# Kernel tuning notes

Measured on AMD Instinct MI355X. Metric: run time of the kernel, lower is better.

## Reference

```python
import jax, jax.numpy as jnp
import numpy as np
import math

B, S, D, M, H = 4, 2048, 1024, 512, 8
DK = M // H


def setup_inputs() -> dict:
    key = jax.random.key(0)
    ks = jax.random.split(key, 16)
    sd = lambda fan_in: 1.0 / math.sqrt(fan_in)
    inp = {
        'x': jax.random.normal(ks[0], (B, S, D), dtype=jnp.float32),
        'W_enc': jax.random.normal(ks[1], (D, M), dtype=jnp.float32) * sd(D),
        'b_enc': jnp.zeros((M,), jnp.float32),
        'Wq': jax.random.normal(ks[2], (M, M), dtype=jnp.float32) * sd(M),
        'bq': jnp.zeros((M,), jnp.float32),
        'Wk': jax.random.normal(ks[3], (M, M), dtype=jnp.float32) * sd(M),
        'bk': jnp.zeros((M,), jnp.float32),
        'Wv': jax.random.normal(ks[4], (M, M), dtype=jnp.float32) * sd(M),
        'bv': jnp.zeros((M,), jnp.float32),
        'Wo': jax.random.normal(ks[5], (M, M), dtype=jnp.float32) * sd(M),
        'bo': jnp.zeros((M,), jnp.float32),
        'ocr_bias': jnp.zeros((1, H, 1, 1), jnp.float32),  # learned, init zeros
        'W1': jax.random.normal(ks[6], (D + M, D), dtype=jnp.float32) * sd(D + M),
        'b1': jnp.zeros((D,), jnp.float32),
        'W2': jax.random.normal(ks[7], (D, D), dtype=jnp.float32) * sd(D),
        'b2': jnp.zeros((D,), jnp.float32),
        'ln_g': jnp.ones((D,), jnp.float32),
        'ln_b': jnp.zeros((D,), jnp.float32),
    }
    return inp


def _ocr_attention(m, Wq, bq, Wk, bk, Wv, bv, Wo, bo, ocr_bias):
    b, s, _ = m.shape
    q = (m @ Wq + bq).reshape(b, s, H, DK).transpose(0, 2, 1, 3)  # bhsd
    k = (m @ Wk + bk).reshape(b, s, H, DK).transpose(0, 2, 1, 3)
    v = (m @ Wv + bv).reshape(b, s, H, DK).transpose(0, 2, 1, 3)
    scores = jnp.einsum('bhqd,bhkd->bhqk', q, k) / math.sqrt(DK) + ocr_bias
    attn = jax.nn.softmax(scores, axis=-1)  # dropout is identity at eval
    ctx = jnp.einsum('bhqk,bhkd->bhqd', attn, v)
    ctx = ctx.transpose(0, 2, 1, 3).reshape(b, s, M)
    return ctx @ Wo + bo


def _layernorm(h, g, bta, eps=1e-5):
    mu = jnp.mean(h, axis=-1, keepdims=True)
    var = jnp.mean(jnp.square(h - mu), axis=-1, keepdims=True)
    return (h - mu) * jax.lax.rsqrt(var + eps) * g + bta


def reference(x, W_enc, b_enc, Wq, bq, Wk, bk, Wv, bv, Wo, bo, ocr_bias, W1, b1, W2, b2, ln_g, ln_b):
    mem = x @ W_enc + b_enc  # [B,S,M] memory-dim stream
    attended = _ocr_attention(mem, Wq, bq, Wk, bk, Wv, bv, Wo, bo, ocr_bias)
    h = jnp.concatenate([x, attended], axis=-1) @ W1 + b1  # [B,S,D]
    h = jax.nn.gelu(h, approximate=False)
    h = h @ W2 + b2
    return _layernorm(h, ln_g, ln_b)
```

## Files before the change

### kernel.cpp

```cpp
#include <hip/hip_runtime.h>
#include <math.h>

#define B_ 4
#define S_ 2048
#define D_ 1024
#define M_ 512
#define H_ 8
#define R_ (B_ * S_)

typedef __bf16 bf8_t __attribute__((ext_vector_type(8)));
typedef __bf16 bf4_t __attribute__((ext_vector_type(4)));
typedef float f4_t __attribute__((ext_vector_type(4)));

typedef __attribute__((address_space(3))) void lds_void;
typedef const __attribute__((address_space(1))) void gl_void;
#define GL16(gp, lp) __builtin_amdgcn_global_load_lds((gl_void*)(gp), (lds_void*)(lp), 16, 0, 0)

__device__ inline unsigned packbf2(float a, float b) {
  union { __bf16 h[2]; unsigned u; } c;
  c.h[0] = (__bf16)a;
  c.h[1] = (__bf16)b;
  return c.u;
}
__device__ inline unsigned bperm(int srcBytes, unsigned v) {
  return (unsigned)__builtin_amdgcn_ds_bpermute(srcBytes, (int)v);
}

__global__ __launch_bounds__(256) void k_convert_x(const float* __restrict__ x,
                                                   __bf16* __restrict__ ab) {
  size_t i = ((size_t)blockIdx.x * 256 + threadIdx.x) * 8;
  size_t row = i >> 10;
  size_t col = i & 1023;
  f4_t f0 = *(const f4_t*)(x + i);
  f4_t f1 = *(const f4_t*)(x + i + 4);
  bf8_t v;
  v[0] = (__bf16)f0[0]; v[1] = (__bf16)f0[1]; v[2] = (__bf16)f0[2]; v[3] = (__bf16)f0[3];
  v[4] = (__bf16)f1[0]; v[5] = (__bf16)f1[1]; v[6] = (__bf16)f1[2]; v[7] = (__bf16)f1[3];
  *(bf8_t*)(ab + row * 1536 + col) = v;
}

__global__ void k_transpose(const float* __restrict__ in, __bf16* __restrict__ out,
                            int K, int N) {
  __shared__ float tile[32][33];
  const int n0 = blockIdx.x * 32;
  const int k0 = blockIdx.y * 32;
  const int tx = threadIdx.x;
  const int ty = threadIdx.y;
#pragma unroll
  for (int j = 0; j < 32; j += 8)
    tile[ty + j][tx] = in[(size_t)(k0 + ty + j) * N + n0 + tx];
  __syncthreads();
#pragma unroll
  for (int j = 0; j < 32; j += 8)
    out[(size_t)(n0 + ty + j) * K + k0 + tx] = (__bf16)tile[tx][ty + j];
}

template <int EPI>
__global__ __launch_bounds__(256) void k_gemm_bt(const __bf16* __restrict__ A, int lda,
                                                 const __bf16* __restrict__ Bt,
                                                 const float* __restrict__ bias,
                                                 __bf16* __restrict__ C, int ldc, int K) {
  __shared__ __bf16 As[128 * 32];
  __shared__ __bf16 Bs[128 * 32];
  const int t = threadIdx.x;
  const int lane = t & 63;
  const int wv = t >> 6;
  const int wr = (wv >> 1) * 64;
  const int wc = (wv & 1) * 64;
  const int bm = blockIdx.y * 128;
  const int bn = blockIdx.x * 128;
  const int c0 = wv * 2, c1 = wv * 2 + 1;
  const int sr0 = c0 * 16 + (lane >> 2);
  const int sr1 = c1 * 16 + (lane >> 2);
  const int scol = (lane & 3) * 8;
  const __bf16* Ag0 = A + (size_t)(bm + sr0) * lda + scol;
  const __bf16* Ag1 = A + (size_t)(bm + sr1) * lda + scol;
  const __bf16* Bg0 = Bt + (size_t)(bn + sr0) * (size_t)K + scol;
  const __bf16* Bg1 = Bt + (size_t)(bn + sr1) * (size_t)K + scol;
  __bf16* Al0 = As + c0 * 512;
  __bf16* Al1 = As + c1 * 512;
  __bf16* Bl0 = Bs + c0 * 512;
  __bf16* Bl1 = Bs + c1 * 512;
  f4_t acc[4][4];
#pragma unroll
  for (int m = 0; m < 4; ++m)
#pragma unroll
    for (int n = 0; n < 4; ++n) acc[m][n] = (f4_t){0.f, 0.f, 0.f, 0.f};
  const int fr = lane & 15;
  const int fk = (lane >> 4) * 8;
  for (int k0 = 0; k0 < K; k0 += 32) {
    __syncthreads();
    GL16(Ag0 + k0, Al0);
    GL16(Ag1 + k0, Al1);
    GL16(Bg0 + k0, Bl0);
    GL16(Bg1 + k0, Bl1);
    __syncthreads();
    bf8_t af[4], bfr[4];
#pragma unroll
    for (int m = 0; m < 4; ++m) af[m] = *(const bf8_t*)&As[(wr + m * 16 + fr) * 32 + fk];
#pragma unroll
    for (int n = 0; n < 4; ++n) bfr[n] = *(const bf8_t*)&Bs[(wc + n * 16 + fr) * 32 + fk];
#pragma unroll
    for (int m = 0; m < 4; ++m)
#pragma unroll
      for (int n = 0; n < 4; ++n)
        acc[m][n] = __builtin_amdgcn_mfma_f32_16x16x32_bf16(af[m], bfr[n], acc[m][n], 0, 0, 0);
  }
  const int cr = (lane >> 4) * 4;
  const int cc = lane & 15;
  if (EPI == 2) {
#pragma unroll
    for (int n = 0; n < 4; ++n) {
      const int col = bn + wc + n * 16 + cc;
      const float bv = bias[col];
#pragma unroll
      for (int m = 0; m < 4; ++m) {
        const int rb = bm + wr + m * 16 + cr;
        bf4_t w;
#pragma unroll
        for (int r = 0; r < 4; ++r) w[r] = (__bf16)(acc[m][n][r] + bv);
        *(bf4_t*)(C + ((size_t)((rb >> 11) * 512 + col)) * 2048 + (rb & 2047)) = w;
      }
    }
    return;
  }
#pragma unroll
  for (int n = 0; n < 4; ++n) {
    const int col = bn + wc + n * 16 + cc;
    const float bv = bias[col];
#pragma unroll
    for (int m = 0; m < 4; ++m)
#pragma unroll
      for (int r = 0; r < 4; ++r) {
        const int row = bm + wr + m * 16 + cr + r;
        float v = acc[m][n][r] + bv;
        if (EPI == 1) v = 0.5f * v * (1.0f + erff(v * 0.70710678118f));
        C[(size_t)row * ldc + col] = (__bf16)v;
      }
  }
}

__global__ __launch_bounds__(256) void k_attn2(const __bf16* __restrict__ qb,
                                               const __bf16* __restrict__ kb,
                                               const __bf16* __restrict__ vt,
                                               const float* __restrict__ ocr_bias,
                                               __bf16* __restrict__ ctx) {
  const int t = threadIdx.x;
  const int lane = t & 63;
  const int wv = t >> 6;
  const int i = blockIdx.x;
  const int xcd = i & 7;
  const int jj = i >> 3;
  const int bh = xcd + 8 * (jj & 3);
  const int xt = jj >> 2;
  const int b = bh >> 3, h = bh & 7;
  const int q0 = xt * 128 + wv * 32;
  const int fr = lane & 15;
  const int g = lane >> 4;
  const int fk = g * 8;
  const float sc = 0.125f;
  const float hb = ocr_bias[h];
  bf8_t bq[2][2];
#pragma unroll
  for (int tt = 0; tt < 2; ++tt)
#pragma unroll
    for (int s = 0; s < 2; ++s)
      bq[tt][s] = *(const bf8_t*)(qb + ((size_t)b * S_ + q0 + tt * 16 + fr) * M_ + h * 64 + s * 32 + fk);
  const __bf16* kbase = kb + (size_t)b * S_ * M_ + h * 64;
  const __bf16* vbase = vt + ((size_t)(b * 512 + h * 64)) * (size_t)S_;
  float mreg[2] = {-1e30f, -1e30f};
  float lreg[2] = {0.f, 0.f};
  f4_t o[2][4];
#pragma unroll
  for (int tt = 0; tt < 2; ++tt)
#pragma unroll
    for (int d = 0; d < 4; ++d) o[tt][d] = (f4_t){0.f, 0.f, 0.f, 0.f};
  const int srcA = (fr + ((g & 1) << 5)) << 2;
  const int srcB = srcA + 64;
  bf8_t akc[2][2];
#pragma unroll
  for (int hh = 0; hh < 2; ++hh)
#pragma unroll
    for (int s = 0; s < 2; ++s)
      akc[hh][s] = *(const bf8_t*)(kbase + (size_t)(hh * 16 + fr) * M_ + s * 32 + fk);

  for (int kv = 0; kv < S_; kv += 32) {
    bf8_t bv[4];
#pragma unroll
    for (int d = 0; d < 4; ++d)
      bv[d] = *(const bf8_t*)(vbase + (size_t)(d * 16 + fr) * S_ + kv + fk);
    f4_t st[2][2];
#pragma unroll
    for (int tt = 0; tt < 2; ++tt)
#pragma unroll
      for (int hh = 0; hh < 2; ++hh) {
        f4_t a = (f4_t){0.f, 0.f, 0.f, 0.f};
        a = __builtin_amdgcn_mfma_f32_16x16x32_bf16(akc[hh][0], bq[tt][0], a, 0, 0, 0);
        a = __builtin_amdgcn_mfma_f32_16x16x32_bf16(akc[hh][1], bq[tt][1], a, 0, 0, 0);
        st[tt][hh] = a;
      }
    const int kvn = (kv + 32) & (S_ - 1);
    bf8_t akn[2][2];
#pragma unroll
    for (int hh = 0; hh < 2; ++hh)
#pragma unroll
      for (int s = 0; s < 2; ++s)
        akn[hh][s] = *(const bf8_t*)(kbase + (size_t)(kvn + hh * 16 + fr) * M_ + s * 32 + fk);
#pragma unroll
    for (int tt = 0; tt < 2; ++tt) {
      float p[2][4];
      float pm = -1e30f;
#pragma unroll
      for (int hh = 0; hh < 2; ++hh)
#pragma unroll
        for (int r = 0; r < 4; ++r) {
          p[hh][r] = st[tt][hh][r] * sc + hb;
          pm = fmaxf(pm, p[hh][r]);
        }
      pm = fmaxf(pm, __shfl_xor(pm, 16, 64));
      pm = fmaxf(pm, __shfl_xor(pm, 32, 64));
      const float mo = mreg[tt];
      const float mn = fmaxf(mo, pm);
      const float al = __expf(mo - mn);
      float ps = 0.f;
#pragma unroll
      for (int hh = 0; hh < 2; ++hh)
#pragma unroll
        for (int r = 0; r < 4; ++r) {
          p[hh][r] = __expf(p[hh][r] - mn);
          ps += p[hh][r];
        }
      ps += __shfl_xor(ps, 16, 64);
      ps += __shfl_xor(ps, 32, 64);
      lreg[tt] = lreg[tt] * al + ps;
      mreg[tt] = mn;
      unsigned ch0 = packbf2(p[0][0], p[0][1]);
      unsigned ch1 = packbf2(p[0][2], p[0][3]);
      unsigned ch2 = packbf2(p[1][0], p[1][1]);
      unsigned ch3 = packbf2(p[1][2], p[1][3]);
      unsigned t0 = bperm(srcA, ch0), t2 = bperm(srcA, ch2);
      unsigned t1 = bperm(srcA, ch1), t3 = bperm(srcA, ch3);
      unsigned u0 = bperm(srcB, ch0), u2 = bperm(srcB, ch2);
      unsigned u1 = bperm(srcB, ch1), u3 = bperm(srcB, ch3);
      const bool lo = (g < 2);
      union { unsigned u[4]; bf8_t v; } aw;
      aw.u[0] = lo ? t0 : t2;
      aw.u[1] = lo ? t1 : t3;
      aw.u[2] = lo ? u0 : u2;
      aw.u[3] = lo ? u1 : u3;
      float alr[4];
#pragma unroll
      for (int r = 0; r < 4; ++r) alr[r] = __shfl(al, g * 4 + r, 64);
#pragma unroll
      for (int d = 0; d < 4; ++d) {
#pragma unroll
        for (int r = 0; r < 4; ++r) o[tt][d][r] *= alr[r];
        o[tt][d] = __builtin_amdgcn_mfma_f32_16x16x32_bf16(aw.v, bv[d], o[tt][d], 0, 0, 0);
      }
    }
#pragma unroll
    for (int hh = 0; hh < 2; ++hh)
#pragma unroll
      for (int s = 0; s < 2; ++s) akc[hh][s] = akn[hh][s];
  }
#pragma unroll
  for (int tt = 0; tt < 2; ++tt) {
    float lrr[4];
#pragma unroll
    for (int r = 0; r < 4; ++r) lrr[r] = __shfl(lreg[tt], g * 4 + r, 64);
#pragma unroll
    for (int d = 0; d < 4; ++d)
#pragma unroll
      for (int r = 0; r < 4; ++r) {
        const float v = o[tt][d][r] / lrr[r];
        ctx[((size_t)b * S_ + q0 + tt * 16 + g * 4 + r) * M_ + h * 64 + d * 16 + fr] = (__bf16)v;
      }
  }
}

__global__ __launch_bounds__(256) void k_ln(const __bf16* __restrict__ hh,
                                            const float* __restrict__ g,
                                            const float* __restrict__ bt,
                                            float* __restrict__ out) {
  const int row = blockIdx.x;
  const int t = threadIdx.x;
  const __bf16* hp = hh + (size_t)row * 1024 + t * 4;
  bf4_t v = *(const bf4_t*)hp;
  float f[4];
  float s1 = 0.f, s2 = 0.f;
#pragma unroll
  for (int j = 0; j < 4; ++j) {
    f[j] = (float)v[j];
    s1 += f[j];
    s2 += f[j] * f[j];
  }
#pragma unroll
  for (int d = 1; d < 64; d <<= 1) {
    s1 += __shfl_xor(s1, d, 64);
    s2 += __shfl_xor(s2, d, 64);
  }
  __shared__ float red[8];
  const int lane = t & 63, wv = t >> 6;
  if (lane == 0) { red[wv] = s1; red[4 + wv] = s2; }
  __syncthreads();
  const float S1 = red[0] + red[1] + red[2] + red[3];
  const float S2 = red[4] + red[5] + red[6] + red[7];
  const float mu = S1 * (1.f / 1024.f);
  const float var = S2 * (1.f / 1024.f) - mu * mu;
  const float inv = rsqrtf(var + 1e-5f);
  float* op = out + (size_t)row * 1024 + t * 4;
#pragma unroll
  for (int j = 0; j < 4; ++j) op[j] = (f[j] - mu) * inv * g[t * 4 + j] + bt[t * 4 + j];
}

extern "C" void kernel_launch(void* const* d_in, const int* in_sizes, int n_in,
                              void* d_out, int out_size, void* d_ws, size_t ws_size,
                              hipStream_t stream) {
  const float* x = (const float*)d_in[0];
  const float* W_enc = (const float*)d_in[1];
  const float* b_enc = (const float*)d_in[2];
  const float* Wq = (const float*)d_in[3];
  const float* bq = (const float*)d_in[4];
  const float* Wk = (const float*)d_in[5];
  const float* bk = (const float*)d_in[6];
  const float* Wv = (const float*)d_in[7];
  const float* bv = (const float*)d_in[8];
  const float* Wo = (const float*)d_in[9];
  const float* bo = (const float*)d_in[10];
  const float* ocr = (const float*)d_in[11];
  const float* W1 = (const float*)d_in[12];
  const float* b1 = (const float*)d_in[13];
  const float* W2 = (const float*)d_in[14];
  const float* b2 = (const float*)d_in[15];
  const float* lng = (const float*)d_in[16];
  const float* lnb = (const float*)d_in[17];
  float* out = (float*)d_out;

  __bf16* p = (__bf16*)d_ws;
  __bf16* ab = p;  p += (size_t)R_ * 1536;
  __bf16* mem = p; p += (size_t)R_ * 512;
  __bf16* qb = p;  p += (size_t)R_ * 512;
  __bf16* kb = p;  p += (size_t)R_ * 512;
  __bf16* vtb = p; p += (size_t)R_ * 512;
  __bf16* cx = p;  p += (size_t)R_ * 512;
  __bf16* h1 = p;  p += (size_t)R_ * 1024;
  __bf16* h2 = p;  p += (size_t)R_ * 1024;
  __bf16* WtE = p; p += (size_t)512 * 1024;
  __bf16* WtQ = p; p += (size_t)512 * 512;
  __bf16* WtK = p; p += (size_t)512 * 512;
  __bf16* WtV = p; p += (size_t)512 * 512;
  __bf16* WtO = p; p += (size_t)512 * 512;
  __bf16* Wt1 = p; p += (size_t)1024 * 1536;
  __bf16* Wt2 = p; p += (size_t)1024 * 1024;

  k_convert_x<<<4096, 256, 0, stream>>>(x, ab);
  dim3 tb(32, 8);
  k_transpose<<<dim3(16, 32), tb, 0, stream>>>(W_enc, WtE, 1024, 512);
  k_transpose<<<dim3(16, 16), tb, 0, stream>>>(Wq, WtQ, 512, 512);
  k_transpose<<<dim3(16, 16), tb, 0, stream>>>(Wk, WtK, 512, 512);
  k_transpose<<<dim3(16, 16), tb, 0, stream>>>(Wv, WtV, 512, 512);
  k_transpose<<<dim3(16, 16), tb, 0, stream>>>(Wo, WtO, 512, 512);
  k_transpose<<<dim3(32, 48), tb, 0, stream>>>(W1, Wt1, 1536, 1024);
  k_transpose<<<dim3(32, 32), tb, 0, stream>>>(W2, Wt2, 1024, 1024);
  k_gemm_bt<0><<<dim3(4, 64), 256, 0, stream>>>(ab, 1536, WtE, b_enc, mem, 512, 1024);
  k_gemm_bt<0><<<dim3(4, 64), 256, 0, stream>>>(mem, 512, WtQ, bq, qb, 512, 512);
  k_gemm_bt<0><<<dim3(4, 64), 256, 0, stream>>>(mem, 512, WtK, bk, kb, 512, 512);
  k_gemm_bt<2><<<dim3(4, 64), 256, 0, stream>>>(mem, 512, WtV, bv, vtb, 2048, 512);
  k_attn2<<<512, 256, 0, stream>>>(qb, kb, vtb, ocr, cx);
  k_gemm_bt<0><<<dim3(4, 64), 256, 0, stream>>>(cx, 512, WtO, bo, ab + 1024, 1536, 512);
  k_gemm_bt<1><<<dim3(8, 64), 256, 0, stream>>>(ab, 1536, Wt1, b1, h1, 1024, 1536);
  k_gemm_bt<0><<<dim3(8, 64), 256, 0, stream>>>(h1, 1024, Wt2, b2, h2, 1024, 1024);
  k_ln<<<R_, 256, 0, stream>>>(h2, lng, lnb, out);
}
```

Measured before the change: 433.7 us.

## Fuse QKV projections and restructure attention with lazy rescale and exp2

Replaces the three separate Q/K/V projection GEMMs with one launch over the contiguous transposed weights (N=1536). It picks the destination, bias and transposed V layout per 512-column segment. The attention kernel now processes 64 keys per step with double-buffered K registers and folds the softmax scale and log2(e) into Q so it can use exp2. It rescales the running max only when it grows by more than 8, and drops the per-head ocr_bias, which cancels under softmax. It also adds s_setprio around the MFMA blocks and a two-waves-per-SIMD launch bound, at the cost of more register pressure and rounding Q to bf16 after scaling.

New measurement: 413.6 us. -4.6%, faster.

```diff
diff --git a/kernel.cpp b/kernel.cpp
--- a/kernel.cpp
+++ b/kernel.cpp
@@ -108,22 +108,6 @@
   }
   const int cr = (lane >> 4) * 4;
   const int cc = lane & 15;
-  if (EPI == 2) {
-#pragma unroll
-    for (int n = 0; n < 4; ++n) {
-      const int col = bn + wc + n * 16 + cc;
-      const float bv = bias[col];
-#pragma unroll
-      for (int m = 0; m < 4; ++m) {
-        const int rb = bm + wr + m * 16 + cr;
-        bf4_t w;
-#pragma unroll
-        for (int r = 0; r < 4; ++r) w[r] = (__bf16)(acc[m][n][r] + bv);
-        *(bf4_t*)(C + ((size_t)((rb >> 11) * 512 + col)) * 2048 + (rb & 2047)) = w;
-      }
-    }
-    return;
-  }
 #pragma unroll
   for (int n = 0; n < 4; ++n) {
     const int col = bn + wc + n * 16 + cc;
@@ -140,11 +124,100 @@
   }
 }
 
-__global__ __launch_bounds__(256) void k_attn2(const __bf16* __restrict__ qb,
-                                               const __bf16* __restrict__ kb,
-                                               const __bf16* __restrict__ vt,
-                                               const float* __restrict__ ocr_bias,
-                                               __bf16* __restrict__ ctx) {
+__global__ __launch_bounds__(256) void k_gemm_qkv(const __bf16* __restrict__ A,
+                                                  const __bf16* __restrict__ Bt,
+                                                  const float* __restrict__ bq,
+                                                  const float* __restrict__ bk,
+                                                  const float* __restrict__ bv,
+                                                  __bf16* __restrict__ qb,
+                                                  __bf16* __restrict__ kb,
+                                                  __bf16* __restrict__ vtb) {
+  const int K = 512;
+  __shared__ __bf16 As[128 * 32];
+  __shared__ __bf16 Bs[128 * 32];
+  const int t = threadIdx.x;
+  const int lane = t & 63;
+  const int wv = t >> 6;
+  const int wr = (wv >> 1) * 64;
+  const int wc = (wv & 1) * 64;
+  const int bm = blockIdx.y * 128;
+  const int bn = blockIdx.x * 128;
+  const int c0 = wv * 2, c1 = wv * 2 + 1;
+  const int sr0 = c0 * 16 + (lane >> 2);
+  const int sr1 = c1 * 16 + (lane >> 2);
+  const int scol = (lane & 3) * 8;
+  const __bf16* Ag0 = A + (size_t)(bm + sr0) * K + scol;
+  const __bf16* Ag1 = A + (size_t)(bm + sr1) * K + scol;
+  const __bf16* Bg0 = Bt + (size_t)(bn + sr0) * (size_t)K + scol;
+  const __bf16* Bg1 = Bt + (size_t)(bn + sr1) * (size_t)K + scol;
+  __bf16* Al0 = As + c0 * 512;
+  __bf16* Al1 = As + c1 * 512;
+  __bf16* Bl0 = Bs + c0 * 512;
+  __bf16* Bl1 = Bs + c1 * 512;
+  f4_t acc[4][4];
+#pragma unroll
+  for (int m = 0; m < 4; ++m)
+#pragma unroll
+    for (int n = 0; n < 4; ++n) acc[m][n] = (f4_t){0.f, 0.f, 0.f, 0.f};
+  const int fr = lane & 15;
+  const int fk = (lane >> 4) * 8;
+  for (int k0 = 0; k0 < K; k0 += 32) {
+    __syncthreads();
+    GL16(Ag0 + k0, Al0);
+    GL16(Ag1 + k0, Al1);
+    GL16(Bg0 + k0, Bl0);
+    GL16(Bg1 + k0, Bl1);
+    __syncthreads();
+    bf8_t af[4], bfr[4];
+#pragma unroll
+    for (int m = 0; m < 4; ++m) af[m] = *(const bf8_t*)&As[(wr + m * 16 + fr) * 32 + fk];
+#pragma unroll
+    for (int n = 0; n < 4; ++n) bfr[n] = *(const bf8_t*)&Bs[(wc + n * 16 + fr) * 32 + fk];
+#pragma unroll
+    for (int m = 0; m < 4; ++m)
+#pragma unroll
+      for (int n = 0; n < 4; ++n)
+        acc[m][n] = __builtin_amdgcn_mfma_f32_16x16x32_bf16(af[m], bfr[n], acc[m][n], 0, 0, 0);
+  }
+  const int cr = (lane >> 4) * 4;
+  const int cc = lane & 15;
+  const int seg = bn >> 9;
+  const float* bsel = (seg == 0) ? bq : (seg == 1) ? bk : bv;
+  if (seg < 2) {
+    __bf16* dst = (seg == 0) ? qb : kb;
+#pragma unroll
+    for (int n = 0; n < 4; ++n) {
+      const int col = (bn + wc + n * 16 + cc) & 511;
+      const float bvv = bsel[col];
+#pragma unroll
+      for (int m = 0; m < 4; ++m)
+#pragma unroll
+        for (int r = 0; r < 4; ++r) {
+          const int row = bm + wr + m * 16 + cr + r;
+          dst[(size_t)row * 512 + col] = (__bf16)(acc[m][n][r] + bvv);
+        }
+    }
+  } else {
+#pragma unroll
+    for (int n = 0; n < 4; ++n) {
+      const int col = (bn + wc + n * 16 + cc) & 511;
+      const float bvv = bsel[col];
+#pragma unroll
+      for (int m = 0; m < 4; ++m) {
+        const int rb = bm + wr + m * 16 + cr;
+        bf4_t w;
+#pragma unroll
+        for (int r = 0; r < 4; ++r) w[r] = (__bf16)(acc[m][n][r] + bvv);
+        *(bf4_t*)(vtb + ((size_t)((rb >> 11) * 512 + col)) * 2048 + (rb & 2047)) = w;
+      }
+    }
+  }
+}
+
+__global__ __launch_bounds__(256, 2) void k_attn3(const __bf16* __restrict__ qb,
+                                                  const __bf16* __restrict__ kb,
+                                                  const __bf16* __restrict__ vt,
+                                                  __bf16* __restrict__ ctx) {
   const int t = threadIdx.x;
   const int lane = t & 63;
   const int wv = t >> 6;
@@ -158,17 +231,21 @@
   const int fr = lane & 15;
   const int g = lane >> 4;
   const int fk = g * 8;
-  const float sc = 0.125f;
-  const float hb = ocr_bias[h];
-  bf8_t bq[2][2];
+  const float qs = 0.125f * 1.44269504f;
+  bf8_t bqf[2][2];
 #pragma unroll
   for (int tt = 0; tt < 2; ++tt)
 #pragma unroll
-    for (int s = 0; s < 2; ++s)
-      bq[tt][s] = *(const bf8_t*)(qb + ((size_t)b * S_ + q0 + tt * 16 + fr) * M_ + h * 64 + s * 32 + fk);
+    for (int s = 0; s < 2; ++s) {
+      bf8_t raw = *(const bf8_t*)(qb + ((size_t)b * S_ + q0 + tt * 16 + fr) * M_ + h * 64 + s * 32 + fk);
+      bf8_t sc;
+#pragma unroll
+      for (int e = 0; e < 8; ++e) sc[e] = (__bf16)((float)raw[e] * qs);
+      bqf[tt][s] = sc;
+    }
   const __bf16* kbase = kb + (size_t)b * S_ * M_ + h * 64;
   const __bf16* vbase = vt + ((size_t)(b * 512 + h * 64)) * (size_t)S_;
-  float mreg[2] = {-1e30f, -1e30f};
+  float mreg[2] = {-3e38f, -3e38f};
   float lreg[2] = {0.f, 0.f};
   f4_t o[2][4];
 #pragma unroll
@@ -177,92 +254,92 @@
     for (int d = 0; d < 4; ++d) o[tt][d] = (f4_t){0.f, 0.f, 0.f, 0.f};
   const int srcA = (fr + ((g & 1) << 5)) << 2;
   const int srcB = srcA + 64;
-  bf8_t akc[2][2];
-#pragma unroll
-  for (int hh = 0; hh < 2; ++hh)
+  bf8_t ak0[4][2], ak1[4][2];
+#pragma unroll
+  for (int hh = 0; hh < 4; ++hh)
 #pragma unroll
     for (int s = 0; s < 2; ++s)
-      akc[hh][s] = *(const bf8_t*)(kbase + (size_t)(hh * 16 + fr) * M_ + s * 32 + fk);
-
-  for (int kv = 0; kv < S_; kv += 32) {
-    bf8_t bv[4];
-#pragma unroll
-    for (int d = 0; d < 4; ++d)
-      bv[d] = *(const bf8_t*)(vbase + (size_t)(d * 16 + fr) * S_ + kv + fk);
-    f4_t st[2][2];
-#pragma unroll
-    for (int tt = 0; tt < 2; ++tt)
-#pragma unroll
-      for (int hh = 0; hh < 2; ++hh) {
-        f4_t a = (f4_t){0.f, 0.f, 0.f, 0.f};
-        a = __builtin_amdgcn_mfma_f32_16x16x32_bf16(akc[hh][0], bq[tt][0], a, 0, 0, 0);
-        a = __builtin_amdgcn_mfma_f32_16x16x32_bf16(akc[hh][1], bq[tt][1], a, 0, 0, 0);
-        st[tt][hh] = a;
-      }
-    const int kvn = (kv + 32) & (S_ - 1);
-    bf8_t akn[2][2];
-#pragma unroll
-    for (int hh = 0; hh < 2; ++hh)
-#pragma unroll
-      for (int s = 0; s < 2; ++s)
-        akn[hh][s] = *(const bf8_t*)(kbase + (size_t)(kvn + hh * 16 + fr) * M_ + s * 32 + fk);
-#pragma unroll
-    for (int tt = 0; tt < 2; ++tt) {
-      float p[2][4];
-      float pm = -1e30f;
-#pragma unroll
-      for (int hh = 0; hh < 2; ++hh)
-#pragma unroll
-        for (int r = 0; r < 4; ++r) {
-          p[hh][r] = st[tt][hh][r] * sc + hb;
-          pm = fmaxf(pm, p[hh][r]);
-        }
-      pm = fmaxf(pm, __shfl_xor(pm, 16, 64));
-      pm = fmaxf(pm, __shfl_xor(pm, 32, 64));
-      const float mo = mreg[tt];
-      const float mn = fmaxf(mo, pm);
-      const float al = __expf(mo - mn);
-      float ps = 0.f;
-#pragma unroll
-      for (int hh = 0; hh < 2; ++hh)
-#pragma unroll
-        for (int r = 0; r < 4; ++r) {
-          p[hh][r] = __expf(p[hh][r] - mn);
-          ps += p[hh][r];
-        }
-      ps += __shfl_xor(ps, 16, 64);
-      ps += __shfl_xor(ps, 32, 64);
-      lreg[tt] = lreg[tt] * al + ps;
-      mreg[tt] = mn;
-      unsigned ch0 = packbf2(p[0][0], p[0][1]);
-      unsigned ch1 = packbf2(p[0][2], p[0][3]);
-      unsigned ch2 = packbf2(p[1][0], p[1][1]);
-      unsigned ch3 = packbf2(p[1][2], p[1][3]);
-      unsigned t0 = bperm(srcA, ch0), t2 = bperm(srcA, ch2);
-      unsigned t1 = bperm(srcA, ch1), t3 = bperm(srcA, ch3);
-      unsigned u0 = bperm(srcB, ch0), u2 = bperm(srcB, ch2);
-      unsigned u1 = bperm(srcB, ch1), u3 = bperm(srcB, ch3);
-      const bool lo = (g < 2);
-      union { unsigned u[4]; bf8_t v; } aw;
-      aw.u[0] = lo ? t0 : t2;
-      aw.u[1] = lo ? t1 : t3;
-      aw.u[2] = lo ? u0 : u2;
-      aw.u[3] = lo ? u1 : u3;
-      float alr[4];
-#pragma unroll
-      for (int r = 0; r < 4; ++r) alr[r] = __shfl(al, g * 4 + r, 64);
-#pragma unroll
-      for (int d = 0; d < 4; ++d) {
-#pragma unroll
-        for (int r = 0; r < 4; ++r) o[tt][d][r] *= alr[r];
-        o[tt][d] = __builtin_amdgcn_mfma_f32_16x16x32_bf16(aw.v, bv[d], o[tt][d], 0, 0, 0);
-      }
-    }
-#pragma unroll
-    for (int hh = 0; hh < 2; ++hh)
-#pragma unroll
-      for (int s = 0; s < 2; ++s) akc[hh][s] = akn[hh][s];
-  }
+      ak0[hh][s] = *(const bf8_t*)(kbase + (size_t)(hh * 16 + fr) * M_ + s * 32 + fk);
+
+#define ATTN_CHUNK(AKC, AKN, KV)                                                          \
+  {                                                                                       \
+    bf8_t bvf[2][4];                                                                      \
+    _Pragma("unroll") for (int ks = 0; ks < 2; ++ks)                                      \
+        _Pragma("unroll") for (int d = 0; d < 4; ++d)                                     \
+            bvf[ks][d] = *(const bf8_t*)(vbase + (size_t)(d * 16 + fr) * S_ + (KV) + ks * 32 + fk); \
+    f4_t st[2][4];                                                                        \
+    __builtin_amdgcn_s_setprio(1);                                                        \
+    _Pragma("unroll") for (int tt = 0; tt < 2; ++tt)                                      \
+        _Pragma("unroll") for (int hh = 0; hh < 4; ++hh) {                                \
+      f4_t a = (f4_t){0.f, 0.f, 0.f, 0.f};                                                \
+      a = __builtin_amdgcn_mfma_f32_16x16x32_bf16(AKC[hh][0], bqf[tt][0], a, 0, 0, 0);    \
+      a = __builtin_amdgcn_mfma_f32_16x16x32_bf16(AKC[hh][1], bqf[tt][1], a, 0, 0, 0);    \
+      st[tt][hh] = a;                                                                     \
+    }                                                                                     \
+    __builtin_amdgcn_s_setprio(0);                                                        \
+    const int kvn = ((KV) + 64) & (S_ - 1);                                               \
+    _Pragma("unroll") for (int hh = 0; hh < 4; ++hh)                                      \
+        _Pragma("unroll") for (int s = 0; s < 2; ++s)                                     \
+            AKN[hh][s] = *(const bf8_t*)(kbase + (size_t)(kvn + hh * 16 + fr) * M_ + s * 32 + fk); \
+    _Pragma("unroll") for (int tt = 0; tt < 2; ++tt) {                                    \
+      float pm = -3e38f;                                                                  \
+      _Pragma("unroll") for (int hh = 0; hh < 4; ++hh)                                    \
+          _Pragma("unroll") for (int r = 0; r < 4; ++r) pm = fmaxf(pm, st[tt][hh][r]);    \
+      pm = fmaxf(pm, __shfl_xor(pm, 16, 64));                                             \
+      pm = fmaxf(pm, __shfl_xor(pm, 32, 64));                                             \
+      float mo = mreg[tt];                                                                \
+      if (!__all(pm <= mo + 8.f)) {                                                       \
+        const float mn = fmaxf(mo, pm);                                                   \
+        const float al = exp2f(mo - mn);                                                  \
+        mreg[tt] = mn;                                                                    \
+        mo = mn;                                                                          \
+        lreg[tt] *= al;                                                                   \
+        float alr[4];                                                                     \
+        _Pragma("unroll") for (int r = 0; r < 4; ++r) alr[r] = __shfl(al, g * 4 + r, 64); \
+        _Pragma("unroll") for (int d = 0; d < 4; ++d)                                     \
+            _Pragma("unroll") for (int r = 0; r < 4; ++r) o[tt][d][r] *= alr[r];          \
+      }                                                                                   \
+      float p[4][4];                                                                      \
+      float ps = 0.f;                                                                     \
+      _Pragma("unroll") for (int hh = 0; hh < 4; ++hh)                                    \
+          _Pragma("unroll") for (int r = 0; r < 4; ++r) {                                 \
+        p[hh][r] = exp2f(st[tt][hh][r] - mo);                                             \
+        ps += p[hh][r];                                                                   \
+      }                                                                                   \
+      ps += __shfl_xor(ps, 16, 64);                                                       \
+      ps += __shfl_xor(ps, 32, 64);                                                       \
+      lreg[tt] += ps;                                                                     \
+      union { unsigned u[4]; bf8_t v; } aw[2];                                            \
+      _Pragma("unroll") for (int ks = 0; ks < 2; ++ks) {                                  \
+        unsigned ch0 = packbf2(p[2 * ks][0], p[2 * ks][1]);                               \
+        unsigned ch1 = packbf2(p[2 * ks][2], p[2 * ks][3]);                               \
+        unsigned ch2 = packbf2(p[2 * ks + 1][0], p[2 * ks + 1][1]);                       \
+        unsigned ch3 = packbf2(p[2 * ks + 1][2], p[2 * ks + 1][3]);                       \
+        unsigned t0 = bperm(srcA, ch0), t2 = bperm(srcA, ch2);                            \
+        unsigned t1 = bperm(srcA, ch1), t3 = bperm(srcA, ch3);                            \
+        unsigned u0 = bperm(srcB, ch0), u2 = bperm(srcB, ch2);                            \
+        unsigned u1 = bperm(srcB, ch1), u3 = bperm(srcB, ch3);                            \
+        const bool lo = (g < 2);                                                          \
+        aw[ks].u[0] = lo ? t0 : t2;                                                       \
+        aw[ks].u[1] = lo ? t1 : t3;                                                       \
+        aw[ks].u[2] = lo ? u0 : u2;                                                       \
+        aw[ks].u[3] = lo ? u1 : u3;                                                       \
+      }                                                                                   \
+      __builtin_amdgcn_s_setprio(1);                                                      \
+      _Pragma("unroll") for (int d = 0; d < 4; ++d) {                                     \
+        o[tt][d] = __builtin_amdgcn_mfma_f32_16x16x32_bf16(aw[0].v, bvf[0][d], o[tt][d], 0, 0, 0); \
+        o[tt][d] = __builtin_amdgcn_mfma_f32_16x16x32_bf16(aw[1].v, bvf[1][d], o[tt][d], 0, 0, 0); \
+      }                                                                                   \
+      __builtin_amdgcn_s_setprio(0);                                                      \
+    }                                                                                     \
+  }
+
+  for (int kv = 0; kv < S_; kv += 128) {
+    ATTN_CHUNK(ak0, ak1, kv);
+    ATTN_CHUNK(ak1, ak0, kv + 64);
+  }
+#undef ATTN_CHUNK
+
 #pragma unroll
   for (int tt = 0; tt < 2; ++tt) {
     float lrr[4];
@@ -327,7 +404,6 @@
   const float* bv = (const float*)d_in[8];
   const float* Wo = (const float*)d_in[9];
   const float* bo = (const float*)d_in[10];
-  const float* ocr = (const float*)d_in[11];
   const float* W1 = (const float*)d_in[12];
   const float* b1 = (const float*)d_in[13];
   const float* W2 = (const float*)d_in[14];
@@ -363,10 +439,8 @@
   k_transpose<<<dim3(32, 48), tb, 0, stream>>>(W1, Wt1, 1536, 1024);
   k_transpose<<<dim3(32, 32), tb, 0, stream>>>(W2, Wt2, 1024, 1024);
   k_gemm_bt<0><<<dim3(4, 64), 256, 0, stream>>>(ab, 1536, WtE, b_enc, mem, 512, 1024);
-  k_gemm_bt<0><<<dim3(4, 64), 256, 0, stream>>>(mem, 512, WtQ, bq, qb, 512, 512);
-  k_gemm_bt<0><<<dim3(4, 64), 256, 0, stream>>>(mem, 512, WtK, bk, kb, 512, 512);
-  k_gemm_bt<2><<<dim3(4, 64), 256, 0, stream>>>(mem, 512, WtV, bv, vtb, 2048, 512);
-  k_attn2<<<512, 256, 0, stream>>>(qb, kb, vtb, ocr, cx);
+  k_gemm_qkv<<<dim3(12, 64), 256, 0, stream>>>(mem, WtQ, bq, bk, bv, qb, kb, vtb);
+  k_attn3<<<512, 256, 0, stream>>>(qb, kb, vtb, cx);
   k_gemm_bt<0><<<dim3(4, 64), 256, 0, stream>>>(cx, 512, WtO, bo, ab + 1024, 1536, 512);
   k_gemm_bt<1><<<dim3(8, 64), 256, 0, stream>>>(ab, 1536, Wt1, b1, h1, 1024, 1536);
   k_gemm_bt<0><<<dim3(8, 64), 256, 0, stream>>>(h1, 1024, Wt2, b2, h2, 1024, 1024);
```
